# Kernel optimization log

Hardware: AMD Instinct MI355X
Metric: run time of the kernel (lower is better)

## Reference

```python
import jax, jax.numpy as jnp
import numpy as np
from jax import lax

B, H, W = 8, 512, 512


def setup_inputs() -> dict:
    key = jax.random.key(0)
    k1, k2, k3, k4, k5 = jax.random.split(key, 5)
    img = jax.random.uniform(k1, (B, 3, H, W), jnp.float32)
    omega = 0.8 + 0.15 * jax.random.uniform(k2, (B, 1), jnp.float32)
    atmospheric_light = 0.5 + 0.5 * jax.random.uniform(k3, (B, 3), jnp.float32)
    L_low = 2.0 * jax.random.uniform(k4, (B, 1), jnp.float32)          # percent in [0,2)
    L_high = 95.0 + 4.0 * jax.random.uniform(k5, (B, 1), jnp.float32)  # percent in [95,99)
    guided_radius = 15  # python int, uniform across batch (original clamps to [1,50])
    return {"img": img, "omega": omega, "atmospheric_light": atmospheric_light,
            "L_low": L_low, "L_high": L_high, "guided_radius": guided_radius}


def _box_filter(x, r):
    # reflect-pad + mean over (2r+1)x(2r+1) window, separable (exactly avg_pool2d on reflect-padded input)
    k = 2 * r + 1
    xp = jnp.pad(x, ((0, 0), (0, 0), (r, r), (r, r)), mode='reflect')
    s = lax.reduce_window(xp, 0.0, lax.add, (1, 1, k, 1), (1, 1, 1, 1), 'VALID')
    s = lax.reduce_window(s, 0.0, lax.add, (1, 1, 1, k), (1, 1, 1, 1), 'VALID')
    return s / (k * k)


def _forward(img, omega, atmospheric_light, L_low, L_high, r):
    eps = 0.5
    Bb, Cc, Hh, Ww = img.shape
    A = atmospheric_light.reshape(Bb, 3, 1, 1)
    # initial transmission: t = 1 - omega * min_c(I/A)
    dark = jnp.min(img / (A + 1e-8), axis=1, keepdims=True)           # (B,1,H,W)
    t0 = 1.0 - omega.reshape(Bb, 1, 1, 1) * dark
    # gradient constraint (weights from t0, applied to shifted copies)
    wx = jnp.exp(-jnp.abs(t0[:, :, :, 1:] - t0[:, :, :, :-1]))
    tx = jnp.concatenate([t0[:, :, :, :1], t0[:, :, :, :-1] * wx], axis=3)
    wy = jnp.exp(-jnp.abs(t0[:, :, 1:, :] - t0[:, :, :-1, :]))
    tg = jnp.concatenate([tx[:, :, :1, :], tx[:, :, :-1, :] * wy], axis=2)
    # guided filter with grayscale guide
    rgb_w = jnp.array([0.299, 0.587, 0.114], dtype=img.dtype).reshape(1, 3, 1, 1)
    gray = jnp.sum(img * rgb_w, axis=1, keepdims=True)                # (B,1,H,W)
    mI = _box_filter(gray, r)
    mp = _box_filter(tg, r)
    mIp = _box_filter(gray * tg, r)
    cov_Ip = mIp - mI * mp
    var_I = _box_filter(gray * gray, r) - mI * mI
    a = cov_Ip / (var_I + eps)
    b = mp - a * mI
    t_final = jnp.clip(_box_filter(a, r) * gray + _box_filter(b, r), 0.1, 1.0)
    # restoration
    J = jnp.clip((img - A) / (t_final + 1e-8) + A, 0.0, 1.0)
    # percentile color stretch (vectorized over B and C)
    n = Hh * Ww
    svals = jnp.sort(J.reshape(Bb, Cc, n), axis=-1)
    li = jnp.clip((L_low / 100.0 * n).astype(jnp.int32), 0, n - 1)    # (B,1)
    hi = jnp.clip((L_high / 100.0 * n).astype(jnp.int32), 0, n - 1)
    p_low = jnp.take_along_axis(svals, jnp.broadcast_to(li[:, :, None], (Bb, Cc, 1)), axis=-1).reshape(Bb, Cc, 1, 1)
    p_high = jnp.take_along_axis(svals, jnp.broadcast_to(hi[:, :, None], (Bb, Cc, 1)), axis=-1).reshape(Bb, Cc, 1, 1)
    out = (jnp.clip(J, p_low, p_high) - p_low) / (p_high - p_low + 1e-8)
    return jnp.clip(out, 0.0, 1.0)


def reference(img, omega, atmospheric_light, L_low, L_high, guided_radius):
    r = max(1, min(int(guided_radius), 50))
    return _forward(img, omega, atmospheric_light, L_low, L_high, r)
```

## Files before the change

kernel.cpp:

```cpp
#include <hip/hip_runtime.h>
#include <cstdint>

constexpr int Bb = 8, Hh = 512, Ww = 512;
constexpr int HWn = Hh * Ww;
constexpr int CH1  = 8;
constexpr int CH23 = 8;
constexpr int CHK4 = 4;
constexpr int NBIN = 1024;
constexpr int NCHK = Hh / 8;

__device__ __forceinline__ int reflect_idx(int p, int n) {
    p = (p < 0) ? -p : p;
    return (p < n) ? p : (2 * n - 2 - p);
}
__device__ __forceinline__ int clamp_r(const int* rad) {
    int r = rad[0];
    return (r < 1) ? 1 : ((r > 50) ? 50 : r);
}
__device__ __forceinline__ float4 f4add(float4 a, float4 b) {
    return make_float4(a.x + b.x, a.y + b.y, a.z + b.z, a.w + b.w);
}
__device__ __forceinline__ float4 f4sub(float4 a, float4 b) {
    return make_float4(a.x - b.x, a.y - b.y, a.z - b.z, a.w - b.w);
}

__device__ __forceinline__ float4 ps_range(const float4* __restrict__ P,
                                           const float4* __restrict__ T,
                                           int a, int b, int pitch) {
    float4 res = P[(size_t)b * pitch];
    int cs;
    if (a > 0) {
        res = f4sub(res, P[(size_t)(a - 1) * pitch]);
        cs = (a - 1) >> 3;
    } else {
        cs = 0;
    }
    const int cb = b >> 3;
    for (int c = cs; c < cb; ++c)
        res = f4add(res, T[(size_t)c * pitch]);
    return res;
}

__device__ __forceinline__ float4 win_sum(const float4* __restrict__ P,
                                          const float4* __restrict__ T,
                                          int y, int r, int pitch) {
    const int lo = y - r, hi = y + r;
    const int a = lo < 0 ? 0 : lo;
    const int b = hi > Hh - 1 ? Hh - 1 : hi;
    float4 s = ps_range(P, T, a, b, pitch);
    if (lo < 0)      s = f4add(s, ps_range(P, T, 1, -lo, pitch));
    if (hi > Hh - 1) s = f4add(s, ps_range(P, T, 2 * Hh - 2 - hi, Hh - 2, pitch));
    return s;
}

__global__ __launch_bounds__(512) void k1_stats_h(
    const float* __restrict__ img, const float* __restrict__ omega,
    const float* __restrict__ atm, const int* __restrict__ rad,
    float4* __restrict__ P1, float4* __restrict__ T1,
    unsigned int* __restrict__ histzero)
{
    const int tile = blockIdx.x;
    const int b = blockIdx.y;
    const int y0 = tile * CH1;
    const int j = threadIdx.x;
    const int fbid = b * gridDim.x + tile;
    if (fbid < 48) histzero[fbid * 512 + j] = 0u;
    const int r = clamp_r(rad);

    __shared__ float t0buf[2][512];
    __shared__ float4 Pb[512];
    __shared__ float4 wsum[8];

    const float om = omega[b];
    const float iA0 = 1.0f / (atm[b*3+0] + 1e-8f);
    const float iA1 = 1.0f / (atm[b*3+1] + 1e-8f);
    const float iA2 = 1.0f / (atm[b*3+2] + 1e-8f);
    const float* imb = img + (size_t)b * 3 * HWn;

    {
        const int yp = (y0 > 0) ? (y0 - 1) : 0;
        float r1 = imb[0*HWn + yp*Ww + j];
        float g1 = imb[1*HWn + yp*Ww + j];
        float b1 = imb[2*HWn + yp*Ww + j];
        t0buf[0][j] = 1.0f - om * fminf(fminf(r1*iA0, g1*iA1), b1*iA2);
    }
    __syncthreads();

    const int lane = j & 63, wv = j >> 6;
    int pv = 0;
    float4 pacc = make_float4(0.f, 0.f, 0.f, 0.f);
    for (int k = 0; k < CH1; ++k) {
        const int y = y0 + k;
        float r0 = imb[0*HWn + y*Ww + j];
        float g0 = imb[1*HWn + y*Ww + j];
        float b0 = imb[2*HWn + y*Ww + j];
        float t0c = 1.0f - om * fminf(fminf(r0*iA0, g0*iA1), b0*iA2);
        float gr = 0.299f*r0 + 0.587f*g0 + 0.114f*b0;
        const float* t0p = t0buf[pv];
        t0buf[pv^1][j] = t0c;
        float tpj = t0p[j];
        float tx  = (j == 0) ? t0p[0] : t0p[j-1] * __expf(-fabsf(tpj - t0p[j-1]));
        float tgv = (y == 0) ? tx : tx * __expf(-fabsf(t0c - tpj));

        float4 incl;
        incl.x = gr; incl.y = tgv; incl.z = gr * tgv; incl.w = gr * gr;
        #pragma unroll
        for (int off = 1; off < 64; off <<= 1) {
            float ux = __shfl_up(incl.x, off);
            float uy = __shfl_up(incl.y, off);
            float uz = __shfl_up(incl.z, off);
            float uw = __shfl_up(incl.w, off);
            if (lane >= off) { incl.x += ux; incl.y += uy; incl.z += uz; incl.w += uw; }
        }
        if (lane == 63) wsum[wv] = incl;
        __syncthreads();
        float4 o4 = make_float4(0.f, 0.f, 0.f, 0.f);
        #pragma unroll
        for (int w = 0; w < 7; ++w) {
            if (w < wv) o4 = f4add(o4, wsum[w]);
        }
        float4 P = f4add(incl, o4);
        Pb[j] = P;
        __syncthreads();

        const int lo = j - r, hi = j + r;
        float4 s = Pb[(hi > 511) ? 511 : hi];
        if (lo > 0)   s = f4sub(s, Pb[lo-1]);
        if (lo < 0)   s = f4add(s, f4sub(Pb[r - j], Pb[0]));
        if (hi > 511) s = f4add(s, f4sub(Pb[510], Pb[1021 - j - r]));

        pacc = f4add(pacc, s);
        P1[((size_t)b * Hh + y) * Ww + j] = pacc;
        pv ^= 1;
    }
    T1[((size_t)b * NCHK + tile) * Ww + j] = pacc;
}

__global__ __launch_bounds__(512) void k23_ab_h(
    const float4* __restrict__ P1, const float4* __restrict__ T1,
    const int* __restrict__ rad,
    float2* __restrict__ P2, float2* __restrict__ T2)
{
    const int b  = blockIdx.y;
    const int y0 = blockIdx.x * CH23;
    const int j  = threadIdx.x;
    const int r  = clamp_r(rad);
    const float ikk = 1.0f / (float)((2*r+1) * (2*r+1));
    const int lane = j & 63, wv = j >> 6;

    __shared__ float2 Pb8[CH23][512];
    __shared__ float2 wsum8[CH23][8];

    const float4* Pj = P1 + (size_t)b * Hh * Ww + j;
    const float4* Tj = T1 + (size_t)b * NCHK * Ww + j;

    float av[CH23], bv[CH23];
    if (r == 15 && y0 >= 16 && y0 <= Hh - 24) {
        const int c0 = y0 >> 3;
        float4 Ta = Tj[(size_t)(c0-2) * Ww];
        float4 Tb = Tj[(size_t)(c0-1) * Ww];
        float4 Tc = Tj[(size_t)(c0  ) * Ww];
        float4 Td = Tj[(size_t)(c0+1) * Ww];
        float4 TTb0 = f4add(f4add(Ta, Tb), Tc);
        float4 TTb1 = f4add(TTb0, Td);
        #pragma unroll
        for (int k = 0; k < CH23; ++k) {
            float4 Phi = Pj[(size_t)(y0 + k + 15) * Ww];
            float4 Plo = Pj[(size_t)(y0 + k - 16) * Ww];
            float4 W = f4sub(f4add(Phi, (k == 0) ? TTb0 : TTb1), Plo);
            float mI = W.x * ikk, mp = W.y * ikk, mIp = W.z * ikk, mII = W.w * ikk;
            float a = (mIp - mI * mp) / (mII - mI * mI + 0.5f);
            av[k] = a;
            bv[k] = mp - a * mI;
        }
    } else {
        for (int k = 0; k < CH23; ++k) {
            float4 W = win_sum(Pj, Tj, y0 + k, r, Ww);
            float mI = W.x * ikk, mp = W.y * ikk, mIp = W.z * ikk, mII = W.w * ikk;
            float a = (mIp - mI * mp) / (mII - mI * mI + 0.5f);
            av[k] = a;
            bv[k] = mp - a * mI;
        }
    }

    float ix[CH23], iy[CH23];
    #pragma unroll
    for (int k = 0; k < CH23; ++k) {
        float sx = av[k], sy = bv[k];
        #pragma unroll
        for (int off = 1; off < 64; off <<= 1) {
            float ux = __shfl_up(sx, off);
            float uy = __shfl_up(sy, off);
            if (lane >= off) { sx += ux; sy += uy; }
        }
        ix[k] = sx; iy[k] = sy;
        if (lane == 63) { wsum8[k][wv].x = sx; wsum8[k][wv].y = sy; }
    }
    __syncthreads();

    #pragma unroll
    for (int k = 0; k < CH23; ++k) {
        float ox = 0.f, oy = 0.f;
        #pragma unroll
        for (int w = 0; w < 7; ++w) {
            if (w < wv) { float2 t = wsum8[k][w]; ox += t.x; oy += t.y; }
        }
        Pb8[k][j].x = ix[k] + ox;
        Pb8[k][j].y = iy[k] + oy;
    }
    __syncthreads();

    const int lo = j - r, hi = j + r;
    const int him = (hi > 511) ? 511 : hi;
    float2 hacc; hacc.x = 0.f; hacc.y = 0.f;
    #pragma unroll
    for (int k = 0; k < CH23; ++k) {
        float2 hs = Pb8[k][him];
        if (lo > 0)   { float2 t = Pb8[k][lo-1];  hs.x -= t.x; hs.y -= t.y; }
        if (lo < 0)   { float2 t = Pb8[k][r-j], u = Pb8[k][0];
                        hs.x += t.x - u.x; hs.y += t.y - u.y; }
        if (hi > 511) { float2 t = Pb8[k][510], u = Pb8[k][1021-j-r];
                        hs.x += t.x - u.x; hs.y += t.y - u.y; }
        hacc.x += hs.x; hacc.y += hs.y;
        P2[((size_t)b * Hh + (y0 + k)) * Ww + j] = hacc;
    }
    T2[((size_t)b * NCHK + (y0 >> 3)) * Ww + j] = hacc;
}

__global__ __launch_bounds__(256) void k4_final_v(
    const float4* __restrict__ P2f4, const float4* __restrict__ T2f4,
    const float2* __restrict__ img2,
    const float* __restrict__ atm, const int* __restrict__ rad,
    float2* __restrict__ J2, unsigned int* __restrict__ hist)
{
    const int b   = blockIdx.y;
    const int y0  = blockIdx.x * CHK4;
    const int tid = threadIdx.x;
    const int r   = clamp_r(rad);
    const float ikk = 1.0f / (float)((2*r+1) * (2*r+1));
    const int HP4 = Ww / 2;
    const int CP2 = HWn / 2;
    const int RP2 = Ww / 2;

    __shared__ unsigned int lh[3 * NBIN];
    for (int i = tid; i < 3 * NBIN; i += 256) lh[i] = 0u;
    __syncthreads();

    const float A0 = atm[b*3+0], A1 = atm[b*3+1], A2 = atm[b*3+2];
    const float2* imb = img2 + (size_t)b * 3 * CP2;
    float2*       Jb  = J2   + (size_t)b * 3 * CP2;
    const float4* Pj  = P2f4 + (size_t)b * Hh * HP4 + tid;
    const float4* Tj  = T2f4 + (size_t)b * NCHK * HP4 + tid;

    float4 Wk[CHK4];
    if (r == 15 && y0 >= 16 && y0 <= Hh - 20) {
        const int c0 = y0 >> 3;
        const int off = y0 & 7;
        float4 Ta = Tj[(size_t)(c0-2) * HP4];
        float4 Tb = Tj[(size_t)(c0-1) * HP4];
        float4 Tc = Tj[(size_t)(c0  ) * HP4];
        float4 Td = Tj[(size_t)(c0+1) * HP4];
        float4 TTb0 = f4add(f4add(Ta, Tb), Tc);
        float4 TTb1 = f4add(TTb0, Td);
        #pragma unroll
        for (int k = 0; k < CHK4; ++k) {
            float4 Phi = Pj[(size_t)(y0 + k + 15) * HP4];
            float4 Plo = Pj[(size_t)(y0 + k - 16) * HP4];
            Wk[k] = f4sub(f4add(Phi, (k == 0 && off == 0) ? TTb0 : TTb1), Plo);
        }
    } else {
        #pragma unroll
        for (int k = 0; k < CHK4; ++k)
            Wk[k] = win_sum(Pj, Tj, y0 + k, r, HP4);
    }

    unsigned int clo0 = 0, chi0 = 0, clo1 = 0, chi1 = 0, clo2 = 0, chi2 = 0;

    #pragma unroll
    for (int k = 0; k < CHK4; ++k) {
        const int y = y0 + k;
        const size_t po = (size_t)y * RP2 + tid;
        float2 c0v = imb[0*CP2 + po];
        float2 c1v = imb[1*CP2 + po];
        float2 c2v = imb[2*CP2 + po];

        float jr[2], jg[2], jb[2];
        {
            float g_ = 0.299f*c0v.x + 0.587f*c1v.x + 0.114f*c2v.x;
            float t  = fminf(fmaxf((Wk[k].x * g_ + Wk[k].y) * ikk, 0.1f), 1.0f);
            float it = 1.0f / (t + 1e-8f);
            jr[0] = fminf(fmaxf((c0v.x - A0) * it + A0, 0.f), 1.f);
            jg[0] = fminf(fmaxf((c1v.x - A1) * it + A1, 0.f), 1.f);
            jb[0] = fminf(fmaxf((c2v.x - A2) * it + A2, 0.f), 1.f);
        }
        {
            float g_ = 0.299f*c0v.y + 0.587f*c1v.y + 0.114f*c2v.y;
            float t  = fminf(fmaxf((Wk[k].z * g_ + Wk[k].w) * ikk, 0.1f), 1.0f);
            float it = 1.0f / (t + 1e-8f);
            jr[1] = fminf(fmaxf((c0v.y - A0) * it + A0, 0.f), 1.f);
            jg[1] = fminf(fmaxf((c1v.y - A1) * it + A1, 0.f), 1.f);
            jb[1] = fminf(fmaxf((c2v.y - A2) * it + A2, 0.f), 1.f);
        }
        Jb[0*CP2 + po] = make_float2(jr[0], jr[1]);
        Jb[1*CP2 + po] = make_float2(jg[0], jg[1]);
        Jb[2*CP2 + po] = make_float2(jb[0], jb[1]);

        #pragma unroll
        for (int q = 0; q < 2; ++q) {
            int bR = (int)(jr[q] * (float)NBIN); bR = (bR > NBIN-1) ? NBIN-1 : bR;
            if (bR == 0) clo0++; else if (bR == NBIN-1) chi0++; else atomicAdd(&lh[0*NBIN + bR], 1u);
            int bG = (int)(jg[q] * (float)NBIN); bG = (bG > NBIN-1) ? NBIN-1 : bG;
            if (bG == 0) clo1++; else if (bG == NBIN-1) chi1++; else atomicAdd(&lh[1*NBIN + bG], 1u);
            int bB = (int)(jb[q] * (float)NBIN); bB = (bB > NBIN-1) ? NBIN-1 : bB;
            if (bB == 0) clo2++; else if (bB == NBIN-1) chi2++; else atomicAdd(&lh[2*NBIN + bB], 1u);
        }
    }

    if (clo0) atomicAdd(&lh[0*NBIN],            clo0);
    if (chi0) atomicAdd(&lh[0*NBIN + NBIN - 1], chi0);
    if (clo1) atomicAdd(&lh[1*NBIN],            clo1);
    if (chi1) atomicAdd(&lh[1*NBIN + NBIN - 1], chi1);
    if (clo2) atomicAdd(&lh[2*NBIN],            clo2);
    if (chi2) atomicAdd(&lh[2*NBIN + NBIN - 1], chi2);
    __syncthreads();

    const size_t hb = (size_t)b * 3 * NBIN;
    for (int i = tid; i < 3 * NBIN; i += 256) {
        unsigned int v = lh[i];
        if (v) atomicAdd(&hist[hb + i], v);
    }
}

__global__ __launch_bounds__(256) void k6_norm(
    float4* __restrict__ J4, const unsigned int* __restrict__ hist,
    const float* __restrict__ L_low, const float* __restrict__ L_high)
{
    const int bc  = blockIdx.x >> 6;
    const int sub = blockIdx.x & 63;
    const int b   = bc / 3;
    __shared__ float sp[2];

    if (threadIdx.x < 64) {
        const int lane = threadIdx.x;
        const unsigned int* hb = hist + (size_t)bc * NBIN;
        unsigned int loc[NBIN / 64];
        unsigned int lsum = 0;
        #pragma unroll
        for (int i = 0; i < NBIN / 64; ++i) { loc[i] = hb[lane * (NBIN/64) + i]; lsum += loc[i]; }
        unsigned int incl = lsum;
        #pragma unroll
        for (int off = 1; off < 64; off <<= 1) {
            unsigned int v = __shfl_up(incl, off);
            if (lane >= off) incl += v;
        }
        unsigned int excl = incl - lsum;
        #pragma unroll
        for (int t = 0; t < 2; ++t) {
            float L = t ? L_high[b] : L_low[b];
            int k = (int)(L * (1.0f / 100.0f) * (float)HWn);
            k = (k < 0) ? 0 : ((k > HWn - 1) ? HWn - 1 : k);
            if ((unsigned int)k >= excl && (unsigned int)k < incl) {
                unsigned int c = excl;
                #pragma unroll
                for (int i = 0; i < NBIN / 64; ++i) {
                    if ((unsigned int)k < c + loc[i]) {
                        sp[t] = ((float)(lane * (NBIN/64) + i) + 0.5f) * (1.0f / (float)NBIN);
                        break;
                    }
                    c += loc[i];
                }
            }
        }
    }
    __syncthreads();

    const float l = sp[0], h = sp[1];
    const float inv = 1.0f / (h - l + 1e-8f);
    float4* base = J4 + (size_t)bc * (HWn / 4) + (size_t)sub * 1024;
    #pragma unroll
    for (int s = 0; s < 4; ++s) {
        const int idx = threadIdx.x + s * 256;
        float4 v = base[idx];
        v.x = fminf(fmaxf((fminf(fmaxf(v.x, l), h) - l) * inv, 0.f), 1.f);
        v.y = fminf(fmaxf((fminf(fmaxf(v.y, l), h) - l) * inv, 0.f), 1.f);
        v.z = fminf(fmaxf((fminf(fmaxf(v.z, l), h) - l) * inv, 0.f), 1.f);
        v.w = fminf(fmaxf((fminf(fmaxf(v.w, l), h) - l) * inv, 0.f), 1.f);
        base[idx] = v;
    }
}

extern "C" void kernel_launch(void* const* d_in, const int* in_sizes, int n_in,
                              void* d_out, int out_size, void* d_ws, size_t ws_size,
                              hipStream_t stream)
{
    const float* img    = (const float*)d_in[0];
    const float* omega  = (const float*)d_in[1];
    const float* atm    = (const float*)d_in[2];
    const float* L_low  = (const float*)d_in[3];
    const float* L_high = (const float*)d_in[4];
    const int*   rad    = (const int*)d_in[5];
    float* J  = (float*)d_out;
    float* ws = (float*)d_ws;

    const size_t F = (size_t)Bb * HWn;
    float4* P1 = (float4*)ws;
    float2* P2 = (float2*)(ws + 4 * F);
    float4* T1 = (float4*)(ws + 6 * F);
    float2* T2 = (float2*)(ws + 6 * F + F / 2);
    unsigned int* hist = (unsigned int*)(ws + 6 * F + F / 2 + F / 4);

    k1_stats_h<<<dim3(Hh/CH1,  Bb), 512, 0, stream>>>(img, omega, atm, rad, P1, T1, hist);
    k23_ab_h  <<<dim3(Hh/CH23, Bb), 512, 0, stream>>>(P1, T1, rad, P2, T2);
    k4_final_v<<<dim3(Hh/CHK4, Bb), 256, 0, stream>>>((const float4*)P2, (const float4*)T2,
                                                      (const float2*)img, atm, rad,
                                                      (float2*)J, hist);
    k6_norm   <<<24 * 64, 256, 0, stream>>>((float4*)J, hist, L_low, L_high);
}
```

Before: 169.4 us.

## Batch k1 row scans four at a time and preload image rows

The first kernel now loads all nine image rows it needs up front, stores their t0 values in shared memory and keeps the gray values in registers. It then processes rows in groups of four, so the wave-level prefix scans and block barriers are shared across four rows instead of two barriers per row. This cuts barrier count and exposes more independent work and memory-level parallelism, at the cost of more shared memory (Pb grows 4x) and higher register pressure, which may lower occupancy.

```diff
diff --git a/kernel.cpp b/kernel.cpp
--- a/kernel.cpp
+++ b/kernel.cpp
@@ -67,9 +67,9 @@
     if (fbid < 48) histzero[fbid * 512 + j] = 0u;
     const int r = clamp_r(rad);
 
-    __shared__ float t0buf[2][512];
-    __shared__ float4 Pb[512];
-    __shared__ float4 wsum[8];
+    __shared__ float  t0a[CH1 + 1][512];
+    __shared__ float4 Pb[4][512];
+    __shared__ float4 wsum[4][8];
 
     const float om = omega[b];
     const float iA0 = 1.0f / (atm[b*3+0] + 1e-8f);
@@ -77,61 +77,72 @@
     const float iA2 = 1.0f / (atm[b*3+2] + 1e-8f);
     const float* imb = img + (size_t)b * 3 * HWn;
 
-    {
-        const int yp = (y0 > 0) ? (y0 - 1) : 0;
-        float r1 = imb[0*HWn + yp*Ww + j];
-        float g1 = imb[1*HWn + yp*Ww + j];
-        float b1 = imb[2*HWn + yp*Ww + j];
-        t0buf[0][j] = 1.0f - om * fminf(fminf(r1*iA0, g1*iA1), b1*iA2);
+    float gr[CH1];
+    #pragma unroll
+    for (int q = 0; q <= CH1; ++q) {
+        int y = y0 + q - 1; if (y < 0) y = 0;
+        float rv = imb[0*HWn + y*Ww + j];
+        float gv = imb[1*HWn + y*Ww + j];
+        float bv = imb[2*HWn + y*Ww + j];
+        t0a[q][j] = 1.0f - om * fminf(fminf(rv*iA0, gv*iA1), bv*iA2);
+        if (q >= 1) gr[q-1] = 0.299f*rv + 0.587f*gv + 0.114f*bv;
     }
     __syncthreads();
 
     const int lane = j & 63, wv = j >> 6;
-    int pv = 0;
+    const int lo = j - r, hi = j + r;
+    const int him = (hi > 511) ? 511 : hi;
     float4 pacc = make_float4(0.f, 0.f, 0.f, 0.f);
-    for (int k = 0; k < CH1; ++k) {
-        const int y = y0 + k;
-        float r0 = imb[0*HWn + y*Ww + j];
-        float g0 = imb[1*HWn + y*Ww + j];
-        float b0 = imb[2*HWn + y*Ww + j];
-        float t0c = 1.0f - om * fminf(fminf(r0*iA0, g0*iA1), b0*iA2);
-        float gr = 0.299f*r0 + 0.587f*g0 + 0.114f*b0;
-        const float* t0p = t0buf[pv];
-        t0buf[pv^1][j] = t0c;
-        float tpj = t0p[j];
-        float tx  = (j == 0) ? t0p[0] : t0p[j-1] * __expf(-fabsf(tpj - t0p[j-1]));
-        float tgv = (y == 0) ? tx : tx * __expf(-fabsf(t0c - tpj));
-
-        float4 incl;
-        incl.x = gr; incl.y = tgv; incl.z = gr * tgv; incl.w = gr * gr;
-        #pragma unroll
-        for (int off = 1; off < 64; off <<= 1) {
-            float ux = __shfl_up(incl.x, off);
-            float uy = __shfl_up(incl.y, off);
-            float uz = __shfl_up(incl.z, off);
-            float uw = __shfl_up(incl.w, off);
-            if (lane >= off) { incl.x += ux; incl.y += uy; incl.z += uz; incl.w += uw; }
-        }
-        if (lane == 63) wsum[wv] = incl;
+
+    #pragma unroll
+    for (int g = 0; g < 2; ++g) {
+        float4 incl[4];
+        #pragma unroll
+        for (int kk = 0; kk < 4; ++kk) {
+            const int k = g * 4 + kk;
+            const int y = y0 + k;
+            float tpm = t0a[k][(j == 0) ? 0 : (j - 1)];
+            float tpj = t0a[k][j];
+            float tcj = t0a[k+1][j];
+            float tx  = (j == 0) ? tpj : tpm * __expf(-fabsf(tpj - tpm));
+            float tgv = (y == 0) ? tx : tx * __expf(-fabsf(tcj - tpj));
+            float gv = gr[k];
+            incl[kk] = make_float4(gv, tgv, gv * tgv, gv * gv);
+            #pragma unroll
+            for (int off = 1; off < 64; off <<= 1) {
+                float ux = __shfl_up(incl[kk].x, off);
+                float uy = __shfl_up(incl[kk].y, off);
+                float uz = __shfl_up(incl[kk].z, off);
+                float uw = __shfl_up(incl[kk].w, off);
+                if (lane >= off) {
+                    incl[kk].x += ux; incl[kk].y += uy;
+                    incl[kk].z += uz; incl[kk].w += uw;
+                }
+            }
+            if (lane == 63) wsum[kk][wv] = incl[kk];
+        }
         __syncthreads();
-        float4 o4 = make_float4(0.f, 0.f, 0.f, 0.f);
-        #pragma unroll
-        for (int w = 0; w < 7; ++w) {
-            if (w < wv) o4 = f4add(o4, wsum[w]);
-        }
-        float4 P = f4add(incl, o4);
-        Pb[j] = P;
+
+        #pragma unroll
+        for (int kk = 0; kk < 4; ++kk) {
+            float4 o4 = make_float4(0.f, 0.f, 0.f, 0.f);
+            #pragma unroll
+            for (int w = 0; w < 7; ++w) {
+                if (w < wv) o4 = f4add(o4, wsum[kk][w]);
+            }
+            Pb[kk][j] = f4add(incl[kk], o4);
+        }
         __syncthreads();
 
-        const int lo = j - r, hi = j + r;
-        float4 s = Pb[(hi > 511) ? 511 : hi];
-        if (lo > 0)   s = f4sub(s, Pb[lo-1]);
-        if (lo < 0)   s = f4add(s, f4sub(Pb[r - j], Pb[0]));
-        if (hi > 511) s = f4add(s, f4sub(Pb[510], Pb[1021 - j - r]));
-
-        pacc = f4add(pacc, s);
-        P1[((size_t)b * Hh + y) * Ww + j] = pacc;
-        pv ^= 1;
+        #pragma unroll
+        for (int kk = 0; kk < 4; ++kk) {
+            float4 s = Pb[kk][him];
+            if (lo > 0)   s = f4sub(s, Pb[kk][lo-1]);
+            if (lo < 0)   s = f4add(s, f4sub(Pb[kk][r - j], Pb[kk][0]));
+            if (hi > 511) s = f4add(s, f4sub(Pb[kk][510], Pb[kk][1021 - j - r]));
+            pacc = f4add(pacc, s);
+            P1[((size_t)b * Hh + (y0 + g * 4 + kk)) * Ww + j] = pacc;
+        }
     }
     T1[((size_t)b * NCHK + tile) * Ww + j] = pacc;
 }
@@ -254,7 +265,7 @@
 
     float4 Wk[CHK4];
     if (r == 15 && y0 >= 16 && y0 <= Hh - 20) {
-        const int c0 = y0 >> 3;
+        const int c0  = y0 >> 3;
         const int off = y0 & 7;
         float4 Ta = Tj[(size_t)(c0-2) * HP4];
         float4 Tb = Tj[(size_t)(c0-1) * HP4];
```

Result: no change. 169.7 us (+0.1%).
